# Kernel tuning notes

Measured on AMD Instinct MI355X. Metric: run time of the kernel, lower is better.

Reference implementation:

```python
import jax, jax.numpy as jnp
import numpy as np

B, L, D = 1, 4096, 1024
N_AR, N_DIFF, D_HEAD = 8, 8, 64
H = N_AR + N_DIFF
ROPE_BASE = 10000.0


def rotate_half(x):
    x1, x2 = jnp.split(x, 2, axis=-1)
    return jnp.concatenate([-x2, x1], axis=-1)


def rope_cos_sin(seq_len, d_head):
    inv_freq = 1.0 / (ROPE_BASE ** (jnp.arange(0, d_head, 2, dtype=jnp.float32) / d_head))
    t = jnp.arange(seq_len, dtype=jnp.float32)
    freqs = t[:, None] * inv_freq[None, :]          # [L, d_head//2]
    emb = jnp.concatenate([freqs, freqs], axis=-1)  # [L, d_head]
    return jnp.cos(emb), jnp.sin(emb)


def setup_inputs() -> dict:
    key = jax.random.key(0)
    ks = jax.random.split(key, 5)
    return {
        "hidden_states": jax.random.normal(ks[0], (B, L, D), dtype=jnp.float32),
        "Wq": jax.random.normal(ks[1], (D, H * D_HEAD), dtype=jnp.float32) * 0.02,
        "Wk": jax.random.normal(ks[2], (D, H * D_HEAD), dtype=jnp.float32) * 0.02,
        "Wv": jax.random.normal(ks[3], (D, H * D_HEAD), dtype=jnp.float32) * 0.02,
        "Wo": jax.random.normal(ks[4], (H * D_HEAD, D), dtype=jnp.float32) * 0.02,
    }


def _attend(q, k, v, mask):
    # q,k,v: [B, h, L, d]; mask: [L, L] additive
    scale = D_HEAD ** -0.5
    scores = jnp.einsum("bhqd,bhkd->bhqk", q, k) * scale + mask
    attn = jax.nn.softmax(scores.astype(jnp.float32), axis=-1).astype(q.dtype)
    return jnp.einsum("bhqk,bhkd->bhqd", attn, v)


def reference(hidden_states, Wq, Wk, Wv, Wo):
    b, l, _ = hidden_states.shape

    def heads(x, W):
        return (x @ W).reshape(b, l, H, D_HEAD).transpose(0, 2, 1, 3)  # [B,H,L,d]

    q = heads(hidden_states, Wq)
    k = heads(hidden_states, Wk)
    v = heads(hidden_states, Wv)

    cos, sin = rope_cos_sin(l, D_HEAD)  # [L, d]
    q = q * cos + rotate_half(q) * sin
    k = k * cos + rotate_half(k) * sin

    neg_inf = jnp.finfo(jnp.float32).min
    causal = jnp.where(jnp.tril(jnp.ones((l, l), dtype=bool)), 0.0, -jnp.inf).astype(jnp.float32)

    out_ar = _attend(q[:, :N_AR], k[:, :N_AR], v[:, :N_AR], causal)
    out_diff = _attend(q[:, N_AR:], k[:, N_AR:], v[:, N_AR:], jnp.zeros((l, l), jnp.float32))

    out = jnp.concatenate([out_ar, out_diff], axis=1)          # [B,H,L,d]
    out = out.transpose(0, 2, 1, 3).reshape(b, l, H * D_HEAD)  # [B,L,H*d]
    return out @ Wo
```

## Files before the change

### kernel.cpp

```cpp
#include <hip/hip_runtime.h>

#define LSEQ 4096
#define DMODEL 1024
#define HTOT 16
#define NAR 8
#define DHEAD 64
#define QKVS 3072

typedef unsigned short u16;
typedef unsigned int u32;
typedef __attribute__((ext_vector_type(8))) short bf16x8;
typedef __attribute__((ext_vector_type(4))) short bf16x4;
typedef __attribute__((ext_vector_type(4))) float f32x4;
typedef __attribute__((ext_vector_type(4))) unsigned int u32x4;

typedef __attribute__((address_space(1))) void gvoid;
typedef __attribute__((address_space(3))) void lvoid;

__device__ __forceinline__ void cp16(const void* g, void* l) {
    __builtin_amdgcn_global_load_lds((gvoid*)(void*)g, (lvoid*)l, 16, 0, 0);
}

__device__ __forceinline__ float bfs(u16 v) { return __uint_as_float((u32)v << 16); }
__device__ __forceinline__ u16 f2bf(float f) {
    u32 x = __float_as_uint(f);
    return (u16)((x + 0x7fffu + ((x >> 16) & 1u)) >> 16);
}
__device__ __forceinline__ u32 packtr(float lo, float hi) {
    return __builtin_amdgcn_perm(__float_as_uint(hi), __float_as_uint(lo), 0x07060302u);
}

__global__ __launch_bounds__(256) void transp_cvt3(
    const float* __restrict__ Wq, const float* __restrict__ Wk,
    const float* __restrict__ Wv, u16* __restrict__ D)
{
    __shared__ u16 T[64][72];
    const float* S = (blockIdx.z == 0) ? Wq : ((blockIdx.z == 1) ? Wk : Wv);
    u16* Dz = D + (size_t)blockIdx.z * 1024 * 1024;
    const int tid = threadIdx.x;
    const int bx = blockIdx.x, by = blockIdx.y;
#pragma unroll
    for (int i = 0; i < 4; ++i) {
        int id = tid + i * 256;
        int fr = id >> 4, fc = id & 15;
        float4 v = *(const float4*)(S + (size_t)(by * 64 + fr) * 1024 + bx * 64 + fc * 4);
        T[fc * 4 + 0][fr] = f2bf(v.x);
        T[fc * 4 + 1][fr] = f2bf(v.y);
        T[fc * 4 + 2][fr] = f2bf(v.z);
        T[fc * 4 + 3][fr] = f2bf(v.w);
    }
    __syncthreads();
#pragma unroll
    for (int i = 0; i < 2; ++i) {
        int id = tid + i * 256;
        int c = id >> 3, g = id & 7;
        *(uint4*)(Dz + (size_t)(bx * 64 + c) * 1024 + by * 64 + g * 8) = *(const uint4*)&T[c][g * 8];
    }
}

__global__ __launch_bounds__(256) void transp_cvt(
    const float* __restrict__ S, u16* __restrict__ D)
{
    __shared__ u16 T[64][72];
    const int tid = threadIdx.x;
    const int bx = blockIdx.x, by = blockIdx.y;
#pragma unroll
    for (int i = 0; i < 4; ++i) {
        int id = tid + i * 256;
        int fr = id >> 4, fc = id & 15;
        float4 v = *(const float4*)(S + (size_t)(by * 64 + fr) * 1024 + bx * 64 + fc * 4);
        T[fc * 4 + 0][fr] = f2bf(v.x);
        T[fc * 4 + 1][fr] = f2bf(v.y);
        T[fc * 4 + 2][fr] = f2bf(v.z);
        T[fc * 4 + 3][fr] = f2bf(v.w);
    }
    __syncthreads();
#pragma unroll
    for (int i = 0; i < 2; ++i) {
        int id = tid + i * 256;
        int c = id >> 3, g = id & 7;
        *(uint4*)(D + (size_t)(bx * 64 + c) * 1024 + by * 64 + g * 8) = *(const uint4*)&T[c][g * 8];
    }
}

__global__ __launch_bounds__(256) void gemm_qkv(
    const float* __restrict__ A, const u16* __restrict__ Bt, u16* __restrict__ C)
{
    __shared__ u16 As[2][128][40];
    __shared__ u16 Bs[2][128][32];
    const int tid = threadIdx.x;
    const int lane = tid & 63, w = tid >> 6;
    const int col = lane & 15, quad = lane >> 4;
    const int bm = blockIdx.y << 7, bn = blockIdx.x << 7;
    const int wm = (w & 1) << 6, wn = (w >> 1) << 6;
    const int sr = lane >> 2, sc = (lane & 3) << 3;
    const int ar0 = tid >> 2, ag = (tid & 3) << 3;
    const f32x4 zero = {0.f, 0.f, 0.f, 0.f};
    f32x4 acc[4][4];
#pragma unroll
    for (int i = 0; i < 4; ++i)
#pragma unroll
        for (int j = 0; j < 4; ++j) acc[i][j] = zero;

    {
#pragma unroll
        for (int i = 0; i < 2; ++i)
            cp16(Bt + (size_t)(bn + w * 32 + i * 16 + sr) * 1024 + sc, &Bs[0][w * 32 + i * 16][0]);
#pragma unroll
        for (int it = 0; it < 2; ++it) {
            const float* ap = A + (size_t)(bm + ar0 + it * 64) * 1024 + ag;
            float4 a0 = *(const float4*)ap;
            float4 a1 = *(const float4*)(ap + 4);
            uint4 pk;
            pk.x = packtr(a0.x, a0.y); pk.y = packtr(a0.z, a0.w);
            pk.z = packtr(a1.x, a1.y); pk.w = packtr(a1.z, a1.w);
            *(uint4*)&As[0][ar0 + it * 64][ag] = pk;
        }
    }

    for (int kc = 0; kc < 32; ++kc) {
        const int cur = kc & 1, nxt = cur ^ 1;
        __syncthreads();
        const bool pre = (kc + 1 < 32);
        float4 a0[2], a1[2];
        if (pre) {
            const int k1 = (kc + 1) * 32;
#pragma unroll
            for (int i = 0; i < 2; ++i)
                cp16(Bt + (size_t)(bn + w * 32 + i * 16 + sr) * 1024 + k1 + sc,
                     &Bs[nxt][w * 32 + i * 16][0]);
#pragma unroll
            for (int it = 0; it < 2; ++it) {
                const float* ap = A + (size_t)(bm + ar0 + it * 64) * 1024 + k1 + ag;
                a0[it] = *(const float4*)ap;
                a1[it] = *(const float4*)(ap + 4);
            }
        }
        bf16x8 af[4], bfr[4];
#pragma unroll
        for (int i = 0; i < 4; ++i) af[i] = *(const bf16x8*)&As[cur][wm + i * 16 + col][quad * 8];
#pragma unroll
        for (int j = 0; j < 4; ++j) bfr[j] = *(const bf16x8*)&Bs[cur][wn + j * 16 + col][quad * 8];
#pragma unroll
        for (int i = 0; i < 4; ++i)
#pragma unroll
            for (int j = 0; j < 4; ++j)
                acc[i][j] = __builtin_amdgcn_mfma_f32_16x16x32_bf16(af[i], bfr[j], acc[i][j], 0, 0, 0);
        if (pre) {
#pragma unroll
            for (int it = 0; it < 2; ++it) {
                uint4 pk;
                pk.x = packtr(a0[it].x, a0[it].y); pk.y = packtr(a0[it].z, a0[it].w);
                pk.z = packtr(a1[it].x, a1[it].y); pk.w = packtr(a1[it].z, a1[it].w);
                *(uint4*)&As[nxt][ar0 + it * 64][ag] = pk;
            }
        }
    }

    if (blockIdx.x < 16) {
        const float scale = (blockIdx.x < 8) ? 0.18033688011112042f : 1.0f;
        const float inv0 = __expf((float)col * -0.2878231366242557f);
        const float inv1 = __expf((float)(16 + col) * -0.2878231366242557f);
#pragma unroll
        for (int i = 0; i < 4; ++i)
#pragma unroll
            for (int r = 0; r < 4; ++r) {
                const float t = (float)(bm + wm + i * 16 + quad * 4 + r);
                float s0, c0, s1, c1;
                __sincosf(t * inv0, &s0, &c0);
                __sincosf(t * inv1, &s1, &c1);
                float a0 = acc[i][0][r], b0 = acc[i][2][r];
                acc[i][0][r] = (a0 * c0 - b0 * s0) * scale;
                acc[i][2][r] = (b0 * c0 + a0 * s0) * scale;
                float a1 = acc[i][1][r], b1 = acc[i][3][r];
                acc[i][1][r] = (a1 * c1 - b1 * s1) * scale;
                acc[i][3][r] = (b1 * c1 + a1 * s1) * scale;
            }
    }
#pragma unroll
    for (int i = 0; i < 4; ++i)
#pragma unroll
        for (int j = 0; j < 4; ++j)
#pragma unroll
            for (int r = 0; r < 4; ++r)
                C[(size_t)(bm + wm + i * 16 + quad * 4 + r) * QKVS + bn + wn + j * 16 + col] =
                    f2bf(acc[i][j][r]);
}

__global__ __launch_bounds__(256) void gemm_out(
    const u16* __restrict__ A, const u16* __restrict__ Bt, float* __restrict__ C)
{
    __shared__ u16 As[2][128][32];
    __shared__ u16 Bs[2][128][32];
    const int tid = threadIdx.x;
    const int lane = tid & 63, w = tid >> 6;
    const int col = lane & 15, quad = lane >> 4;
    const int bm = blockIdx.y << 7, bn = blockIdx.x << 7;
    const int wm = (w & 1) << 6, wn = (w >> 1) << 6;
    const int sr = lane >> 2, sc = (lane & 3) << 3;
    const f32x4 zero = {0.f, 0.f, 0.f, 0.f};
    f32x4 acc[4][4];
#pragma unroll
    for (int i = 0; i < 4; ++i)
#pragma unroll
        for (int j = 0; j < 4; ++j) acc[i][j] = zero;

#pragma unroll
    for (int i = 0; i < 2; ++i) {
        const int r0 = w * 32 + i * 16;
        cp16(A  + (size_t)(bm + r0 + sr) * 1024 + sc, &As[0][r0][0]);
        cp16(Bt + (size_t)(bn + r0 + sr) * 1024 + sc, &Bs[0][r0][0]);
    }

    for (int kc = 0; kc < 32; ++kc) {
        const int cur = kc & 1, nxt = cur ^ 1;
        __syncthreads();
        if (kc + 1 < 32) {
            const int k1 = (kc + 1) * 32;
#pragma unroll
            for (int i = 0; i < 2; ++i) {
                const int r0 = w * 32 + i * 16;
                cp16(A  + (size_t)(bm + r0 + sr) * 1024 + k1 + sc, &As[nxt][r0][0]);
                cp16(Bt + (size_t)(bn + r0 + sr) * 1024 + k1 + sc, &Bs[nxt][r0][0]);
            }
        }
        bf16x8 af[4], bfr[4];
#pragma unroll
        for (int i = 0; i < 4; ++i) af[i] = *(const bf16x8*)&As[cur][wm + i * 16 + col][quad * 8];
#pragma unroll
        for (int j = 0; j < 4; ++j) bfr[j] = *(const bf16x8*)&Bs[cur][wn + j * 16 + col][quad * 8];
#pragma unroll
        for (int i = 0; i < 4; ++i)
#pragma unroll
            for (int j = 0; j < 4; ++j)
                acc[i][j] = __builtin_amdgcn_mfma_f32_16x16x32_bf16(af[i], bfr[j], acc[i][j], 0, 0, 0);
    }
#pragma unroll
    for (int i = 0; i < 4; ++i)
#pragma unroll
        for (int j = 0; j < 4; ++j)
#pragma unroll
            for (int r = 0; r < 4; ++r)
                C[(size_t)(bm + wm + i * 16 + quad * 4 + r) * 1024 + bn + wn + j * 16 + col] =
                    acc[i][j][r];
}

__global__ __launch_bounds__(256) void attn_mfma(
    const u16* __restrict__ QKV, u16* __restrict__ AO)
{
    __shared__ u16 Ks[2][128][64];
    __shared__ u16 Vt[2][64][136];
    const int bid = blockIdx.x;
    int h, qt;
    if (bid < 256) { h = 8 + (bid & 7); qt = bid >> 3; }
    else { int i = bid - 256; h = i & 7; qt = 31 - (i >> 3); }
    const bool causal = (h < NAR);
    const int tid = threadIdx.x;
    const int w = tid >> 6, lane = tid & 63;
    const int col = lane & 15, quad = lane >> 4;
    const int qb = qt * 128;
    const int qr0 = qb + w * 32 + col;
    const int qr1 = qr0 + 16;

    bf16x8 qf[2][2];
#pragma unroll
    for (int s = 0; s < 2; ++s)
#pragma unroll
        for (int ks = 0; ks < 2; ++ks)
            qf[s][ks] = *(const bf16x8*)(QKV + (size_t)(qr0 + s * 16) * QKVS +
                                         h * DHEAD + ks * 32 + quad * 8);

    bf16x4 ones;
    ones[0] = (short)0x3F80; ones[1] = (short)0x3F80;
    ones[2] = (short)0x3F80; ones[3] = (short)0x3F80;

    const f32x4 zero = {0.f, 0.f, 0.f, 0.f};
    f32x4 O[2][5];
#pragma unroll
    for (int s = 0; s < 2; ++s)
#pragma unroll
        for (int nd = 0; nd < 5; ++nd) O[s][nd] = zero;

    const int nch = causal ? (qt + 1) : (LSEQ / 128);
    const int krow = lane >> 3;
    const int kcb = (lane & 7) ^ krow;
    const u16* kbase = QKV + (size_t)krow * QKVS + 1024 + h * DHEAD + kcb * 8;
    const u16* vbase = QKV + (size_t)(lane * 2) * QKVS + 2048 + h * DHEAD + w * 16;

    u32x4 vA0, vA1, vB0, vB1;
    bf16x4 pf[2][8];

#pragma unroll
    for (int i = 0; i < 4; ++i)
        cp16(kbase + (size_t)((i * 4 + w) * 8) * QKVS, &Ks[0][(i * 4 + w) * 8][0]);
    vA0 = *(u32x4*)(vbase);
    vA1 = *(u32x4*)(vbase + 8);
    vB0 = *(u32x4*)(vbase + QKVS);
    vB1 = *(u32x4*)(vbase + QKVS + 8);
    __syncthreads();
#pragma unroll
    for (int j = 0; j < 4; ++j) {
        *(u32*)&Vt[0][w * 16 + 2 * j][lane * 2]         = __builtin_amdgcn_perm(vB0[j], vA0[j], 0x05040100u);
        *(u32*)&Vt[0][w * 16 + 2 * j + 1][lane * 2]     = __builtin_amdgcn_perm(vB0[j], vA0[j], 0x07060302u);
        *(u32*)&Vt[0][w * 16 + 8 + 2 * j][lane * 2]     = __builtin_amdgcn_perm(vB1[j], vA1[j], 0x05040100u);
        *(u32*)&Vt[0][w * 16 + 8 + 2 * j + 1][lane * 2] = __builtin_amdgcn_perm(vB1[j], vA1[j], 0x07060302u);
    }
    if (nch > 1) {
#pragma unroll
        for (int i = 0; i < 4; ++i)
            cp16(kbase + (size_t)(128 + (i * 4 + w) * 8) * QKVS, &Ks[1][(i * 4 + w) * 8][0]);
        const u16* vp = vbase + (size_t)128 * QKVS;
        vA0 = *(u32x4*)(vp);
        vA1 = *(u32x4*)(vp + 8);
        vB0 = *(u32x4*)(vp + QKVS);
        vB1 = *(u32x4*)(vp + QKVS + 8);
    }
    {
        const bool mask = causal && (0 == qt);
#pragma unroll
        for (int hf = 0; hf < 2; ++hf) {
            f32x4 st[2][4];
#pragma unroll
            for (int s = 0; s < 2; ++s)
#pragma unroll
                for (int jj = 0; jj < 4; ++jj) st[s][jj] = zero;
#pragma unroll
            for (int jj = 0; jj < 4; ++jj)
#pragma unroll
                for (int ks = 0; ks < 2; ++ks) {
                    bf16x8 kf = *(const bf16x8*)&Ks[0][(hf * 4 + jj) * 16 + col]
                                                    [((ks * 4 + quad) ^ (col & 7)) * 8];
                    st[0][jj] = __builtin_amdgcn_mfma_f32_16x16x32_bf16(kf, qf[0][ks], st[0][jj], 0, 0, 0);
                    st[1][jj] = __builtin_amdgcn_mfma_f32_16x16x32_bf16(kf, qf[1][ks], st[1][jj], 0, 0, 0);
                }
            if (mask) {
#pragma unroll
                for (int jj = 0; jj < 4; ++jj) {
                    const int kk = (hf * 4 + jj) * 16 + quad * 4;
#pragma unroll
                    for (int r = 0; r < 4; ++r) {
                        if (kk + r > qr0) st[0][jj][r] = -1e30f;
                        if (kk + r > qr1) st[1][jj][r] = -1e30f;
                    }
                }
            }
#pragma unroll
            for (int s = 0; s < 2; ++s)
#pragma unroll
                for (int jj = 0; jj < 4; ++jj) {
                    u32 lo = packtr(__builtin_amdgcn_exp2f(st[s][jj][0]),
                                    __builtin_amdgcn_exp2f(st[s][jj][1]));
                    u32 hi = packtr(__builtin_amdgcn_exp2f(st[s][jj][2]),
                                    __builtin_amdgcn_exp2f(st[s][jj][3]));
                    u32* p = (u32*)&pf[s][hf * 4 + jj];
                    p[0] = lo; p[1] = hi;
                }
        }
    }

    for (int ch = 1; ch < nch; ++ch) {
        const int cur = ch & 1, prv = cur ^ 1;
        __syncthreads();
#pragma unroll
        for (int j = 0; j < 4; ++j) {
            *(u32*)&Vt[cur][w * 16 + 2 * j][lane * 2]         = __builtin_amdgcn_perm(vB0[j], vA0[j], 0x05040100u);
            *(u32*)&Vt[cur][w * 16 + 2 * j + 1][lane * 2]     = __builtin_amdgcn_perm(vB0[j], vA0[j], 0x07060302u);
            *(u32*)&Vt[cur][w * 16 + 8 + 2 * j][lane * 2]     = __builtin_amdgcn_perm(vB1[j], vA1[j], 0x05040100u);
            *(u32*)&Vt[cur][w * 16 + 8 + 2 * j + 1][lane * 2] = __builtin_amdgcn_perm(vB1[j], vA1[j], 0x07060302u);
        }
        if (ch + 1 < nch) {
            const size_t c1 = (size_t)(ch + 1) * 128;
#pragma unroll
            for (int i = 0; i < 4; ++i)
                cp16(kbase + (c1 + (i * 4 + w) * 8) * QKVS, &Ks[prv][(i * 4 + w) * 8][0]);
            const u16* vp = vbase + c1 * QKVS;
            vA0 = *(u32x4*)(vp);
            vA1 = *(u32x4*)(vp + 8);
            vB0 = *(u32x4*)(vp + QKVS);
            vB1 = *(u32x4*)(vp + QKVS + 8);
        }
#pragma unroll
        for (int nd = 0; nd < 4; ++nd)
#pragma unroll
            for (int t = 0; t < 8; ++t) {
                bf16x4 vtf = *(const bf16x4*)&Vt[prv][nd * 16 + col][t * 16 + quad * 4];
                O[0][nd] = __builtin_amdgcn_mfma_f32_16x16x16bf16_1k(vtf, pf[0][t], O[0][nd], 0, 0, 0);
                O[1][nd] = __builtin_amdgcn_mfma_f32_16x16x16bf16_1k(vtf, pf[1][t], O[1][nd], 0, 0, 0);
            }
#pragma unroll
        for (int t = 0; t < 8; ++t) {
            O[0][4] = __builtin_amdgcn_mfma_f32_16x16x16bf16_1k(ones, pf[0][t], O[0][4], 0, 0, 0);
            O[1][4] = __builtin_amdgcn_mfma_f32_16x16x16bf16_1k(ones, pf[1][t], O[1][4], 0, 0, 0);
        }
        const bool mask = causal && (ch == qt);
#pragma unroll
        for (int hf = 0; hf < 2; ++hf) {
            f32x4 st[2][4];
#pragma unroll
            for (int s = 0; s < 2; ++s)
#pragma unroll
                for (int jj = 0; jj < 4; ++jj) st[s][jj] = zero;
#pragma unroll
            for (int jj = 0; jj < 4; ++jj)
#pragma unroll
                for (int ks = 0; ks < 2; ++ks) {
                    bf16x8 kf = *(const bf16x8*)&Ks[cur][(hf * 4 + jj) * 16 + col]
                                                    [((ks * 4 + quad) ^ (col & 7)) * 8];
                    st[0][jj] = __builtin_amdgcn_mfma_f32_16x16x32_bf16(kf, qf[0][ks], st[0][jj], 0, 0, 0);
                    st[1][jj] = __builtin_amdgcn_mfma_f32_16x16x32_bf16(kf, qf[1][ks], st[1][jj], 0, 0, 0);
                }
            if (mask) {
#pragma unroll
                for (int jj = 0; jj < 4; ++jj) {
                    const int kk = ch * 128 + (hf * 4 + jj) * 16 + quad * 4;
#pragma unroll
                    for (int r = 0; r < 4; ++r) {
                        if (kk + r > qr0) st[0][jj][r] = -1e30f;
                        if (kk + r > qr1) st[1][jj][r] = -1e30f;
                    }
                }
            }
#pragma unroll
            for (int s = 0; s < 2; ++s)
#pragma unroll
                for (int jj = 0; jj < 4; ++jj) {
                    u32 lo = packtr(__builtin_amdgcn_exp2f(st[s][jj][0]),
                                    __builtin_amdgcn_exp2f(st[s][jj][1]));
                    u32 hi = packtr(__builtin_amdgcn_exp2f(st[s][jj][2]),
                                    __builtin_amdgcn_exp2f(st[s][jj][3]));
                    u32* p = (u32*)&pf[s][hf * 4 + jj];
                    p[0] = lo; p[1] = hi;
                }
        }
    }

    __syncthreads();
    {
        const int prv = (nch - 1) & 1;
#pragma unroll
        for (int nd = 0; nd < 4; ++nd)
#pragma unroll
            for (int t = 0; t < 8; ++t) {
                bf16x4 vtf = *(const bf16x4*)&Vt[prv][nd * 16 + col][t * 16 + quad * 4];
                O[0][nd] = __builtin_amdgcn_mfma_f32_16x16x16bf16_1k(vtf, pf[0][t], O[0][nd], 0, 0, 0);
                O[1][nd] = __builtin_amdgcn_mfma_f32_16x16x16bf16_1k(vtf, pf[1][t], O[1][nd], 0, 0, 0);
            }
#pragma unroll
        for (int t = 0; t < 8; ++t) {
            O[0][4] = __builtin_amdgcn_mfma_f32_16x16x16bf16_1k(ones, pf[0][t], O[0][4], 0, 0, 0);
            O[1][4] = __builtin_amdgcn_mfma_f32_16x16x16bf16_1k(ones, pf[1][t], O[1][4], 0, 0, 0);
        }
    }
#pragma unroll
    for (int s = 0; s < 2; ++s) {
        const float inv = 1.f / O[s][4][0];
        const int qrow = qr0 + s * 16;
#pragma unroll
        for (int nd = 0; nd < 4; ++nd) {
            ushort4 ov;
            ov.x = f2bf(O[s][nd][0] * inv);
            ov.y = f2bf(O[s][nd][1] * inv);
            ov.z = f2bf(O[s][nd][2] * inv);
            ov.w = f2bf(O[s][nd][3] * inv);
            *(ushort4*)(AO + (size_t)qrow * 1024 + h * DHEAD + nd * 16 + quad * 4) = ov;
        }
    }
}

extern "C" void kernel_launch(void* const* d_in, const int* in_sizes, int n_in,
                              void* d_out, int out_size, void* d_ws, size_t ws_size,
                              hipStream_t stream)
{
    const float* X  = (const float*)d_in[0];
    const float* Wq = (const float*)d_in[1];
    const float* Wk = (const float*)d_in[2];
    const float* Wv = (const float*)d_in[3];
    const float* Wo = (const float*)d_in[4];
    float* out = (float*)d_out;

    u16* Wt  = (u16*)d_ws;
    u16* AOb = (u16*)d_ws;
    u16* QKV = (u16*)d_ws + (size_t)4 * 1024 * 1024;
    u16* Wot = QKV;

    transp_cvt3<<<dim3(16, 16, 3), 256, 0, stream>>>(Wq, Wk, Wv, Wt);
    gemm_qkv<<<dim3(24, 32), 256, 0, stream>>>(X, Wt, QKV);
    attn_mfma<<<512, 256, 0, stream>>>(QKV, AOb);
    transp_cvt<<<dim3(16, 16), 256, 0, stream>>>(Wo, Wot);
    gemm_out<<<dim3(8, 32), 256, 0, stream>>>(AOb, Wot, out);
}
```

Measured before the change: 267.2 us.

## Permute V-transpose LDS layout for 16-byte reads and add MFMA priority hints

The transposed V tile in shared memory drops its padding and uses a permuted column layout, so each lane reads 8 bf16 values (two k-steps) with one 16-byte LDS load instead of two 8-byte loads. The PV step is reordered to consume the low and high halves of each load, with the row-sum MFMAs interleaved. s_setprio is raised around the MFMA blocks, and the inner QK loop order is swapped. The goal is fewer LDS instructions and better issue priority; the unpadded, permuted layout may add bank conflicts on the writes.

```diff
diff --git a/kernel.cpp b/kernel.cpp
--- a/kernel.cpp
+++ b/kernel.cpp
@@ -29,6 +29,9 @@
 __device__ __forceinline__ u32 packtr(float lo, float hi) {
     return __builtin_amdgcn_perm(__float_as_uint(hi), __float_as_uint(lo), 0x07060302u);
 }
+
+#define LOHALF(v) __builtin_shufflevector(v, v, 0, 1, 2, 3)
+#define HIHALF(v) __builtin_shufflevector(v, v, 4, 5, 6, 7)
 
 __global__ __launch_bounds__(256) void transp_cvt3(
     const float* __restrict__ Wq, const float* __restrict__ Wk,
@@ -249,7 +252,7 @@
     const u16* __restrict__ QKV, u16* __restrict__ AO)
 {
     __shared__ u16 Ks[2][128][64];
-    __shared__ u16 Vt[2][64][136];
+    __shared__ u16 Vt[2][64][128];
     const int bid = blockIdx.x;
     int h, qt;
     if (bid < 256) { h = 8 + (bid & 7); qt = bid >> 3; }
@@ -261,6 +264,7 @@
     const int qb = qt * 128;
     const int qr0 = qb + w * 32 + col;
     const int qr1 = qr0 + 16;
+    const int cva = ((lane >> 1) & 3) * 32 + (lane >> 3) * 4 + (lane & 1) * 2;
 
     bf16x8 qf[2][2];
 #pragma unroll
@@ -289,6 +293,90 @@
 
     u32x4 vA0, vA1, vB0, vB1;
     bf16x4 pf[2][8];
+
+#define VT_WRITE(CUR)                                                                              \
+    _Pragma("unroll")                                                                              \
+    for (int j = 0; j < 4; ++j) {                                                                  \
+        *(u32*)&Vt[CUR][w * 16 + 2 * j][cva]         = __builtin_amdgcn_perm(vB0[j], vA0[j], 0x05040100u); \
+        *(u32*)&Vt[CUR][w * 16 + 2 * j + 1][cva]     = __builtin_amdgcn_perm(vB0[j], vA0[j], 0x07060302u); \
+        *(u32*)&Vt[CUR][w * 16 + 8 + 2 * j][cva]     = __builtin_amdgcn_perm(vB1[j], vA1[j], 0x05040100u); \
+        *(u32*)&Vt[CUR][w * 16 + 8 + 2 * j + 1][cva] = __builtin_amdgcn_perm(vB1[j], vA1[j], 0x07060302u); \
+    }
+
+#define PV_STEP(PRV)                                                                               \
+    {                                                                                              \
+        __builtin_amdgcn_s_setprio(1);                                                             \
+        _Pragma("unroll")                                                                          \
+        for (int tp = 0; tp < 4; ++tp) {                                                           \
+            bf16x8 vv[4];                                                                          \
+            _Pragma("unroll")                                                                      \
+            for (int nd = 0; nd < 4; ++nd)                                                         \
+                vv[nd] = *(const bf16x8*)&Vt[PRV][nd * 16 + col][quad * 32 + tp * 8];              \
+            _Pragma("unroll")                                                                      \
+            for (int nd = 0; nd < 4; ++nd) {                                                       \
+                bf16x4 lo = LOHALF(vv[nd]);                                                        \
+                O[0][nd] = __builtin_amdgcn_mfma_f32_16x16x16bf16_1k(lo, pf[0][2 * tp], O[0][nd], 0, 0, 0); \
+                O[1][nd] = __builtin_amdgcn_mfma_f32_16x16x16bf16_1k(lo, pf[1][2 * tp], O[1][nd], 0, 0, 0); \
+            }                                                                                      \
+            O[0][4] = __builtin_amdgcn_mfma_f32_16x16x16bf16_1k(ones, pf[0][2 * tp], O[0][4], 0, 0, 0); \
+            O[1][4] = __builtin_amdgcn_mfma_f32_16x16x16bf16_1k(ones, pf[1][2 * tp], O[1][4], 0, 0, 0); \
+            _Pragma("unroll")                                                                      \
+            for (int nd = 0; nd < 4; ++nd) {                                                       \
+                bf16x4 hi = HIHALF(vv[nd]);                                                        \
+                O[0][nd] = __builtin_amdgcn_mfma_f32_16x16x16bf16_1k(hi, pf[0][2 * tp + 1], O[0][nd], 0, 0, 0); \
+                O[1][nd] = __builtin_amdgcn_mfma_f32_16x16x16bf16_1k(hi, pf[1][2 * tp + 1], O[1][nd], 0, 0, 0); \
+            }                                                                                      \
+            O[0][4] = __builtin_amdgcn_mfma_f32_16x16x16bf16_1k(ones, pf[0][2 * tp + 1], O[0][4], 0, 0, 0); \
+            O[1][4] = __builtin_amdgcn_mfma_f32_16x16x16bf16_1k(ones, pf[1][2 * tp + 1], O[1][4], 0, 0, 0); \
+        }                                                                                          \
+        __builtin_amdgcn_s_setprio(0);                                                             \
+    }
+
+#define S_STEP(KBUF, CH)                                                                           \
+    {                                                                                              \
+        const bool mask = causal && ((CH) == qt);                                                  \
+        _Pragma("unroll")                                                                          \
+        for (int hf = 0; hf < 2; ++hf) {                                                           \
+            f32x4 st[2][4];                                                                        \
+            _Pragma("unroll")                                                                      \
+            for (int s = 0; s < 2; ++s)                                                            \
+                _Pragma("unroll")                                                                  \
+                for (int jj = 0; jj < 4; ++jj) st[s][jj] = zero;                                   \
+            __builtin_amdgcn_s_setprio(1);                                                         \
+            _Pragma("unroll")                                                                      \
+            for (int ks = 0; ks < 2; ++ks)                                                         \
+                _Pragma("unroll")                                                                  \
+                for (int jj = 0; jj < 4; ++jj) {                                                   \
+                    bf16x8 kf = *(const bf16x8*)&Ks[KBUF][(hf * 4 + jj) * 16 + col]                \
+                                                         [((ks * 4 + quad) ^ (col & 7)) * 8];      \
+                    st[0][jj] = __builtin_amdgcn_mfma_f32_16x16x32_bf16(kf, qf[0][ks], st[0][jj], 0, 0, 0); \
+                    st[1][jj] = __builtin_amdgcn_mfma_f32_16x16x32_bf16(kf, qf[1][ks], st[1][jj], 0, 0, 0); \
+                }                                                                                  \
+            __builtin_amdgcn_s_setprio(0);                                                         \
+            if (mask) {                                                                            \
+                _Pragma("unroll")                                                                  \
+                for (int jj = 0; jj < 4; ++jj) {                                                   \
+                    const int kk = (CH) * 128 + (hf * 4 + jj) * 16 + quad * 4;                     \
+                    _Pragma("unroll")                                                              \
+                    for (int r = 0; r < 4; ++r) {                                                  \
+                        if (kk + r > qr0) st[0][jj][r] = -1e30f;                                   \
+                        if (kk + r > qr1) st[1][jj][r] = -1e30f;                                   \
+                    }                                                                              \
+                }                                                                                  \
+            }                                                                                      \
+            _Pragma("unroll")                                                                      \
+            for (int s = 0; s < 2; ++s)                                                            \
+                _Pragma("unroll")                                                                  \
+                for (int jj = 0; jj < 4; ++jj) {                                                   \
+                    u32 plo = packtr(__builtin_amdgcn_exp2f(st[s][jj][0]),                         \
+                                     __builtin_amdgcn_exp2f(st[s][jj][1]));                        \
+                    u32 phi = packtr(__builtin_amdgcn_exp2f(st[s][jj][2]),                         \
+                                     __builtin_amdgcn_exp2f(st[s][jj][3]));                        \
+                    u32* p = (u32*)&pf[s][hf * 4 + jj];                                            \
+                    p[0] = plo; p[1] = phi;                                                        \
+                }                                                                                  \
+        }                                                                                          \
+    }
 
 #pragma unroll
     for (int i = 0; i < 4; ++i)
@@ -298,13 +386,7 @@
     vB0 = *(u32x4*)(vbase + QKVS);
     vB1 = *(u32x4*)(vbase + QKVS + 8);
     __syncthreads();
-#pragma unroll
-    for (int j = 0; j < 4; ++j) {
-        *(u32*)&Vt[0][w * 16 + 2 * j][lane * 2]         = __builtin_amdgcn_perm(vB0[j], vA0[j], 0x05040100u);
-        *(u32*)&Vt[0][w * 16 + 2 * j + 1][lane * 2]     = __builtin_amdgcn_perm(vB0[j], vA0[j], 0x07060302u);
-        *(u32*)&Vt[0][w * 16 + 8 + 2 * j][lane * 2]     = __builtin_amdgcn_perm(vB1[j], vA1[j], 0x05040100u);
-        *(u32*)&Vt[0][w * 16 + 8 + 2 * j + 1][lane * 2] = __builtin_amdgcn_perm(vB1[j], vA1[j], 0x07060302u);
-    }
+    VT_WRITE(0);
     if (nch > 1) {
 #pragma unroll
         for (int i = 0; i < 4; ++i)
@@ -315,59 +397,12 @@
         vB0 = *(u32x4*)(vp + QKVS);
         vB1 = *(u32x4*)(vp + QKVS + 8);
     }
-    {
-        const bool mask = causal && (0 == qt);
-#pragma unroll
-        for (int hf = 0; hf < 2; ++hf) {
-            f32x4 st[2][4];
-#pragma unroll
-            for (int s = 0; s < 2; ++s)
-#pragma unroll
-                for (int jj = 0; jj < 4; ++jj) st[s][jj] = zero;
-#pragma unroll
-            for (int jj = 0; jj < 4; ++jj)
-#pragma unroll
-                for (int ks = 0; ks < 2; ++ks) {
-                    bf16x8 kf = *(const bf16x8*)&Ks[0][(hf * 4 + jj) * 16 + col]
-                                                    [((ks * 4 + quad) ^ (col & 7)) * 8];
-                    st[0][jj] = __builtin_amdgcn_mfma_f32_16x16x32_bf16(kf, qf[0][ks], st[0][jj], 0, 0, 0);
-                    st[1][jj] = __builtin_amdgcn_mfma_f32_16x16x32_bf16(kf, qf[1][ks], st[1][jj], 0, 0, 0);
-                }
-            if (mask) {
-#pragma unroll
-                for (int jj = 0; jj < 4; ++jj) {
-                    const int kk = (hf * 4 + jj) * 16 + quad * 4;
-#pragma unroll
-                    for (int r = 0; r < 4; ++r) {
-                        if (kk + r > qr0) st[0][jj][r] = -1e30f;
-                        if (kk + r > qr1) st[1][jj][r] = -1e30f;
-                    }
-                }
-            }
-#pragma unroll
-            for (int s = 0; s < 2; ++s)
-#pragma unroll
-                for (int jj = 0; jj < 4; ++jj) {
-                    u32 lo = packtr(__builtin_amdgcn_exp2f(st[s][jj][0]),
-                                    __builtin_amdgcn_exp2f(st[s][jj][1]));
-                    u32 hi = packtr(__builtin_amdgcn_exp2f(st[s][jj][2]),
-                                    __builtin_amdgcn_exp2f(st[s][jj][3]));
-                    u32* p = (u32*)&pf[s][hf * 4 + jj];
-                    p[0] = lo; p[1] = hi;
-                }
-        }
-    }
+    S_STEP(0, 0);
 
     for (int ch = 1; ch < nch; ++ch) {
         const int cur = ch & 1, prv = cur ^ 1;
         __syncthreads();
-#pragma unroll
-        for (int j = 0; j < 4; ++j) {
-            *(u32*)&Vt[cur][w * 16 + 2 * j][lane * 2]         = __builtin_amdgcn_perm(vB0[j], vA0[j], 0x05040100u);
-            *(u32*)&Vt[cur][w * 16 + 2 * j + 1][lane * 2]     = __builtin_amdgcn_perm(vB0[j], vA0[j], 0x07060302u);
-            *(u32*)&Vt[cur][w * 16 + 8 + 2 * j][lane * 2]     = __builtin_amdgcn_perm(vB1[j], vA1[j], 0x05040100u);
-            *(u32*)&Vt[cur][w * 16 + 8 + 2 * j + 1][lane * 2] = __builtin_amdgcn_perm(vB1[j], vA1[j], 0x07060302u);
-        }
+        VT_WRITE(cur);
         if (ch + 1 < nch) {
             const size_t c1 = (size_t)(ch + 1) * 128;
 #pragma unroll
@@ -379,77 +414,14 @@
             vB0 = *(u32x4*)(vp + QKVS);
             vB1 = *(u32x4*)(vp + QKVS + 8);
         }
-#pragma unroll
-        for (int nd = 0; nd < 4; ++nd)
-#pragma unroll
-            for (int t = 0; t < 8; ++t) {
-                bf16x4 vtf = *(const bf16x4*)&Vt[prv][nd * 16 + col][t * 16 + quad * 4];
-                O[0][nd] = __builtin_amdgcn_mfma_f32_16x16x16bf16_1k(vtf, pf[0][t], O[0][nd], 0, 0, 0);
-                O[1][nd] = __builtin_amdgcn_mfma_f32_16x16x16bf16_1k(vtf, pf[1][t], O[1][nd], 0, 0, 0);
-            }
-#pragma unroll
-        for (int t = 0; t < 8; ++t) {
-            O[0][4] = __builtin_amdgcn_mfma_f32_16x16x16bf16_1k(ones, pf[0][t], O[0][4], 0, 0, 0);
-            O[1][4] = __builtin_amdgcn_mfma_f32_16x16x16bf16_1k(ones, pf[1][t], O[1][4], 0, 0, 0);
-        }
-        const bool mask = causal && (ch == qt);
-#pragma unroll
-        for (int hf = 0; hf < 2; ++hf) {
-            f32x4 st[2][4];
-#pragma unroll
-            for (int s = 0; s < 2; ++s)
-#pragma unroll
-                for (int jj = 0; jj < 4; ++jj) st[s][jj] = zero;
-#pragma unroll
-            for (int jj = 0; jj < 4; ++jj)
-#pragma unroll
-                for (int ks = 0; ks < 2; ++ks) {
-                    bf16x8 kf = *(const bf16x8*)&Ks[cur][(hf * 4 + jj) * 16 + col]
-                                                    [((ks * 4 + quad) ^ (col & 7)) * 8];
-                    st[0][jj] = __builtin_amdgcn_mfma_f32_16x16x32_bf16(kf, qf[0][ks], st[0][jj], 0, 0, 0);
-                    st[1][jj] = __builtin_amdgcn_mfma_f32_16x16x32_bf16(kf, qf[1][ks], st[1][jj], 0, 0, 0);
-                }
-            if (mask) {
-#pragma unroll
-                for (int jj = 0; jj < 4; ++jj) {
-                    const int kk = ch * 128 + (hf * 4 + jj) * 16 + quad * 4;
-#pragma unroll
-                    for (int r = 0; r < 4; ++r) {
-                        if (kk + r > qr0) st[0][jj][r] = -1e30f;
-                        if (kk + r > qr1) st[1][jj][r] = -1e30f;
-                    }
-                }
-            }
-#pragma unroll
-            for (int s = 0; s < 2; ++s)
-#pragma unroll
-                for (int jj = 0; jj < 4; ++jj) {
-                    u32 lo = packtr(__builtin_amdgcn_exp2f(st[s][jj][0]),
-                                    __builtin_amdgcn_exp2f(st[s][jj][1]));
-                    u32 hi = packtr(__builtin_amdgcn_exp2f(st[s][jj][2]),
-                                    __builtin_amdgcn_exp2f(st[s][jj][3]));
-                    u32* p = (u32*)&pf[s][hf * 4 + jj];
-                    p[0] = lo; p[1] = hi;
-                }
-        }
+        PV_STEP(prv);
+        S_STEP(cur, ch);
     }
 
     __syncthreads();
     {
         const int prv = (nch - 1) & 1;
-#pragma unroll
-        for (int nd = 0; nd < 4; ++nd)
-#pragma unroll
-            for (int t = 0; t < 8; ++t) {
-                bf16x4 vtf = *(const bf16x4*)&Vt[prv][nd * 16 + col][t * 16 + quad * 4];
-                O[0][nd] = __builtin_amdgcn_mfma_f32_16x16x16bf16_1k(vtf, pf[0][t], O[0][nd], 0, 0, 0);
-                O[1][nd] = __builtin_amdgcn_mfma_f32_16x16x16bf16_1k(vtf, pf[1][t], O[1][nd], 0, 0, 0);
-            }
-#pragma unroll
-        for (int t = 0; t < 8; ++t) {
-            O[0][4] = __builtin_amdgcn_mfma_f32_16x16x16bf16_1k(ones, pf[0][t], O[0][4], 0, 0, 0);
-            O[1][4] = __builtin_amdgcn_mfma_f32_16x16x16bf16_1k(ones, pf[1][t], O[1][4], 0, 0, 0);
-        }
+        PV_STEP(prv);
     }
 #pragma unroll
     for (int s = 0; s < 2; ++s) {
@@ -465,6 +437,9 @@
             *(ushort4*)(AO + (size_t)qrow * 1024 + h * DHEAD + nd * 16 + quad * 4) = ov;
         }
     }
+#undef VT_WRITE
+#undef PV_STEP
+#undef S_STEP
 }
 
 extern "C" void kernel_launch(void* const* d_in, const int* in_sizes, int n_in,
```

Measured after the change: 281.9 us. 5.5% more time.
